# Performance work log

Hardware: AMD Instinct MI355X
Metric: run time of the kernel (lower is better)

The kernel has to match this reference:

```python
import jax, jax.numpy as jnp
import numpy as np

DS = 32   # self_obs_dim
DO = 32   # obstacle_obs_dim
D = DS + DO
H = 128   # obstacle_hidden_size
B = 512   # batch_size
A = 16    # num_adv_obs = 2 * num_oppo_obs


def _init_linear(key, fan_in, fan_out):
    kw, kb = jax.random.split(key)
    bound = 1.0 / np.sqrt(fan_in)
    w = jax.random.uniform(kw, (fan_in, fan_out), jnp.float32, -bound, bound)
    b = jax.random.uniform(kb, (fan_out,), jnp.float32, -bound, bound)
    return w, b


def setup_inputs() -> dict:
    key = jax.random.key(0)
    ks = jax.random.split(key, 10)
    obs = jax.random.normal(ks[0], (B, DS), jnp.float32)
    latent = jax.random.normal(ks[1], (B, A, DO), jnp.float32)
    hw1, hb1 = _init_linear(ks[2], D, H)
    hw2, hb2 = _init_linear(ks[3], H, D * H)
    vw1, vb1 = _init_linear(ks[4], H, H)
    vw2, vb2 = _init_linear(ks[5], H, H)
    aw1, ab1 = _init_linear(ks[6], 2 * H, H)
    aw2, ab2 = _init_linear(ks[7], H, H)
    aw3, ab3 = _init_linear(ks[8], H, 1)
    return {
        "obs": obs, "obs_intention_latent": latent,
        "hw1": hw1, "hb1": hb1, "hw2": hw2, "hb2": hb2,
        "vw1": vw1, "vb1": vb1, "vw2": vw2, "vb2": vb2,
        "aw1": aw1, "ab1": ab1, "aw2": aw2, "ab2": ab2,
        "aw3": aw3, "ab3": ab3,
        "num_adv_obs": A, "batch_size": B, "num_groups": 1,
    }


def reference(obs, obs_intention_latent, hw1, hb1, hw2, hb2,
              vw1, vb1, vw2, vb2, aw1, ab1, aw2, ab2, aw3, ab3,
              num_adv_obs, batch_size, num_groups):
    relu = jax.nn.relu
    # flatten opponents (batch-major, matches torch .reshape)
    obs_obstacles = obs_intention_latent.reshape(-1, DO)          # [N, DO]
    # torch .repeat(num_adv_obs, 1) tiles the batch dim
    self_rep = jnp.tile(obs[:, :DS], (num_adv_obs, 1))            # [N, DS]
    mlp_input = jnp.concatenate([self_rep, obs_obstacles], axis=1)  # [N, D]
    # hypernet: per-sample weight [N, D, H]
    h = relu(mlp_input @ hw1 + hb1)
    w = relu(h @ hw2 + hb2).reshape(-1, D, H)
    # per-sample vector-matrix product + tanh
    emb = jnp.tanh(jnp.einsum("nd,ndh->nh", mlp_input, w))        # [N, H]
    # neighbor value MLP
    vals = relu(relu(emb @ vw1 + vb1) @ vw2 + vb2)                # [N, H]
    # attention: concat with per-batch mean embedding
    emb_mean = jnp.mean(emb.reshape(batch_size, -1, H), axis=1)   # [B, H]
    mean_rep = jnp.tile(emb_mean, (num_adv_obs, 1))               # [N, H]
    att_in = jnp.concatenate([emb, mean_rep], axis=1)             # [N, 2H]
    scores = relu(relu(att_in @ aw1 + ab1) @ aw2 + ab2) @ aw3 + ab3  # [N, 1]
    att = jax.nn.softmax(scores.reshape(batch_size, -1), axis=1).reshape(-1, 1)
    weighted = (att * vals).reshape(batch_size, -1, H)
    return jnp.sum(weighted, axis=1)                              # [B, H]
```

## Files before the change

### kernel.cpp

```cpp
#include <hip/hip_runtime.h>
#include <hip/hip_bf16.h>
#include <math.h>

#define BATCH 512
#define NADV  16
#define NROWS (BATCH*NADV)
#define DS    32
#define DO    32
#define DIM   64
#define HID   128
#define WCOLS (DIM*HID)
#define LSTR  136
#define PACK_BLOCKS 276

typedef _Float16 half8 __attribute__((ext_vector_type(8)));
typedef float floatx4 __attribute__((ext_vector_type(4)));

__device__ inline void async_ld16(void* lds, const void* g) {
    __builtin_amdgcn_global_load_lds(
        (const __attribute__((address_space(1))) void*)g,
        (__attribute__((address_space(3))) void*)lds, 16, 0, 0);
}

__global__ __launch_bounds__(256)
void k_prep(const float* __restrict__ obs, const float* __restrict__ latent,
            const float* __restrict__ hw1, const float* __restrict__ hb1,
            const float* __restrict__ hw2, const float* __restrict__ vw1,
            const float* __restrict__ vw2, const float* __restrict__ aw1,
            const float* __restrict__ aw2,
            _Float16* __restrict__ hf,
            _Float16* __restrict__ w2p, _Float16* __restrict__ vw1p,
            _Float16* __restrict__ vw2p, _Float16* __restrict__ aw1p,
            _Float16* __restrict__ aw2p) {
    __shared__ __align__(16) float smem[32 * 132];
    int b = blockIdx.x;
    int tid = threadIdx.x;
    if (b < PACK_BLOCKS) {
        const float* src; _Float16* dst; int N, Kt, jb, kt;
        if (b < 256)      { src = hw2; dst = w2p;  N = WCOLS; Kt = 4; jb = b >> 2; kt = b & 3; }
        else if (b < 260) { src = vw1; dst = vw1p; N = HID;   Kt = 4; jb = 0; kt = b - 256; }
        else if (b < 264) { src = vw2; dst = vw2p; N = HID;   Kt = 4; jb = 0; kt = b - 260; }
        else if (b < 272) { src = aw1; dst = aw1p; N = HID;   Kt = 8; jb = 0; kt = b - 264; }
        else              { src = aw2; dst = aw2p; N = HID;   Kt = 4; jb = 0; kt = b - 272; }
        for (int i = tid; i < 32 * 32; i += 256) {
            int r = i >> 5, c4 = (i & 31) * 4;
            *(float4*)&smem[r * 132 + c4] =
                *(const float4*)(src + (size_t)(kt * 32 + r) * N + jb * 128 + c4);
        }
        __syncthreads();
        for (int i = tid; i < 8 * 64; i += 256) {
            int ctl = i >> 6, lane = i & 63;
            int ct = jb * 8 + ctl;
            int rbase = (lane >> 4) * 8, cc = ctl * 16 + (lane & 15);
            half8 v;
#pragma unroll
            for (int e = 0; e < 8; ++e) v[e] = (_Float16)smem[(rbase + e) * 132 + cc];
            *(half8*)(dst + ((size_t)ct * Kt + kt) * 512 + lane * 8) = v;
        }
    } else {
        int n0 = (b - PACK_BLOCKS) * 16;
        float* xs = smem;
        for (int idx = tid; idx < 16 * DIM; idx += 256) {
            int r = idx >> 6, d = idx & 63;
            int n = n0 + r;
            xs[r * DIM + d] = (d < DS) ? obs[(n & (BATCH - 1)) * DS + d]
                                       : latent[(size_t)n * DO + (d - DS)];
        }
        __syncthreads();
        int j = tid & 127, hh = tid >> 7;
        float acc[8];
        float bb = hb1[j];
#pragma unroll
        for (int r = 0; r < 8; ++r) acc[r] = bb;
        for (int d = 0; d < DIM; ++d) {
            float w = hw1[d * HID + j];
#pragma unroll
            for (int r = 0; r < 8; ++r)
                acc[r] = fmaf(xs[(hh * 8 + r) * DIM + d], w, acc[r]);
        }
#pragma unroll
        for (int r = 0; r < 8; ++r)
            hf[(size_t)(n0 + hh * 8 + r) * HID + j] = (_Float16)fmaxf(acc[r], 0.f);
    }
}

__global__ __launch_bounds__(512, 4)
void k_hyper_mfma(const float* __restrict__ obs, const float* __restrict__ latent,
                  const _Float16* __restrict__ hf, const _Float16* __restrict__ w2p,
                  const float* __restrict__ hb2,
                  _Float16* __restrict__ embf, _Float16* __restrict__ emeanf) {
    __shared__ __align__(16) _Float16 Bs[8][4][512];
    __shared__ float xs[128][68];
    __shared__ float bias_s[64 * 16];
    int b  = blockIdx.x;
    int jt = b & 7;
    int rt = b >> 3;
    int n0 = rt * 128;
    int j0 = jt * 16;
    int tid = threadIdx.x;
    int wave = tid >> 6, lane = tid & 63;
    int l15 = lane & 15, quad = lane >> 4;

    for (int i = tid; i < 128 * 16; i += 512) {
        int r = i >> 4, c4 = (i & 15) * 4;
        float4 v;
        if (c4 < DS) v = *(const float4*)(obs + ((n0 + r) & (BATCH - 1)) * DS + c4);
        else         v = *(const float4*)(latent + (size_t)(n0 + r) * DO + (c4 - DS));
        *(float4*)&xs[r][c4] = v;
    }
    for (int i = tid; i < 64 * 16; i += 512)
        bias_s[i] = hb2[(i >> 4) * HID + j0 + (i & 15)];

    half8 af[4];
    {
        const _Float16* arow = hf + (size_t)(n0 + wave * 16 + l15) * HID;
#pragma unroll
        for (int ks = 0; ks < 4; ++ks)
            af[ks] = *(const half8*)(arow + ks * 32 + quad * 8);
    }

    float emb_acc[4] = {0.f, 0.f, 0.f, 0.f};

    for (int d8 = 0; d8 < 8; ++d8) {
        {
            int ct = (d8 * 8 + wave) * 8 + jt;
            const _Float16* src = w2p + (size_t)ct * 2048 + lane * 8;
            _Float16* dst = &Bs[wave][0][0];
#pragma unroll
            for (int kt = 0; kt < 4; ++kt)
                async_ld16(dst + kt * 512, src + kt * 512);
        }
        __syncthreads();

#pragma unroll
        for (int dd = 0; dd < 8; ++dd) {
            int d = d8 * 8 + dd;
            float bb = bias_s[d * 16 + l15];
            floatx4 acc = {bb, bb, bb, bb};
#pragma unroll
            for (int ks = 0; ks < 4; ++ks) {
                half8 bfr = *(const half8*)&Bs[dd][ks][lane * 8];
                acc = __builtin_amdgcn_mfma_f32_16x16x32_f16(af[ks], bfr, acc, 0, 0, 0);
            }
#pragma unroll
            for (int reg = 0; reg < 4; ++reg) {
                float xv = xs[wave * 16 + quad * 4 + reg][d];
                emb_acc[reg] = fmaf(xv, fmaxf(acc[reg], 0.f), emb_acc[reg]);
            }
        }
        __syncthreads();
    }

    float e[4];
#pragma unroll
    for (int reg = 0; reg < 4; ++reg) {
        e[reg] = tanhf(emb_acc[reg]);
        embf[(size_t)(n0 + wave * 16 + quad * 4 + reg) * HID + j0 + l15] =
            (_Float16)e[reg];
    }
    float s = e[0] + e[1] + e[2] + e[3];
    s += __shfl_xor(s, 16, 64);
    s += __shfl_xor(s, 32, 64);
    if (quad == 0)
        emeanf[(size_t)(rt * 8 + wave) * HID + j0 + l15] = (_Float16)(s * (1.f / 16));
}

__global__ __launch_bounds__(512, 4)
void k_tail(const _Float16* __restrict__ embf, const _Float16* __restrict__ emeanf,
            const _Float16* __restrict__ vw1p, const float* __restrict__ vb1,
            const _Float16* __restrict__ vw2p, const float* __restrict__ vb2,
            const _Float16* __restrict__ aw1p, const float* __restrict__ ab1,
            const _Float16* __restrict__ aw2p, const float* __restrict__ ab2,
            const float* __restrict__ aw3, const float* __restrict__ ab3,
            float* __restrict__ out) {
    __shared__ _Float16 embs[16][LSTR];
    __shared__ _Float16 means[16][LSTR];
    __shared__ _Float16 tAs[16][LSTR];
    __shared__ _Float16 tBs[16][LSTR];
    __shared__ float scr[16][32];
    __shared__ float satt[16];
    __shared__ float att[16];
    int g = blockIdx.x;
    int n0 = g * 16;
    int tid = threadIdx.x;
    int wave = tid >> 6, lane = tid & 63, l15 = lane & 15, quad = lane >> 4;
    int ct = wave;

    {
        int m = tid >> 8, r = (tid >> 4) & 15, c8 = (tid & 15) * 8;
        if (m == 0)
            *(half8*)&embs[r][c8] = *(const half8*)(embf + (size_t)(n0 + r) * HID + c8);
        else
            *(half8*)&means[r][c8] =
                *(const half8*)(emeanf + (size_t)((n0 & 511) + r) * HID + c8);
    }
    __syncthreads();

    half8 av[4], amean[4];
#pragma unroll
    for (int ks = 0; ks < 4; ++ks) {
        av[ks]    = *(const half8*)&embs[l15][ks * 32 + quad * 8];
        amean[ks] = *(const half8*)&means[l15][ks * 32 + quad * 8];
    }

    floatx4 acc;
    {
        float bb = vb1[ct * 16 + l15];
        acc = (floatx4){bb, bb, bb, bb};
    }
#pragma unroll
    for (int ks = 0; ks < 4; ++ks) {
        half8 bfr = *(const half8*)(vw1p + ((size_t)ct * 4 + ks) * 512 + lane * 8);
        acc = __builtin_amdgcn_mfma_f32_16x16x32_f16(av[ks], bfr, acc, 0, 0, 0);
    }
#pragma unroll
    for (int reg = 0; reg < 4; ++reg)
        tAs[quad * 4 + reg][ct * 16 + l15] = (_Float16)fmaxf(acc[reg], 0.f);
    __syncthreads();

    half8 at[4];
#pragma unroll
    for (int ks = 0; ks < 4; ++ks)
        at[ks] = *(const half8*)&tAs[l15][ks * 32 + quad * 8];

    floatx4 vacc;
    {
        float bb = vb2[ct * 16 + l15];
        vacc = (floatx4){bb, bb, bb, bb};
    }
#pragma unroll
    for (int ks = 0; ks < 4; ++ks) {
        half8 bfr = *(const half8*)(vw2p + ((size_t)ct * 4 + ks) * 512 + lane * 8);
        vacc = __builtin_amdgcn_mfma_f32_16x16x32_f16(at[ks], bfr, vacc, 0, 0, 0);
    }

    floatx4 aacc;
    {
        float bb = ab1[ct * 16 + l15];
        aacc = (floatx4){bb, bb, bb, bb};
    }
#pragma unroll
    for (int ks = 0; ks < 8; ++ks) {
        half8 bfr = *(const half8*)(aw1p + ((size_t)ct * 8 + ks) * 512 + lane * 8);
        half8 a = (ks < 4) ? av[ks] : amean[ks - 4];
        aacc = __builtin_amdgcn_mfma_f32_16x16x32_f16(a, bfr, aacc, 0, 0, 0);
    }
#pragma unroll
    for (int reg = 0; reg < 4; ++reg)
        tBs[quad * 4 + reg][ct * 16 + l15] = (_Float16)fmaxf(aacc[reg], 0.f);
    __syncthreads();

    half8 aa[4];
#pragma unroll
    for (int ks = 0; ks < 4; ++ks)
        aa[ks] = *(const half8*)&tBs[l15][ks * 32 + quad * 8];

    floatx4 a2acc;
    {
        float bb = ab2[ct * 16 + l15];
        a2acc = (floatx4){bb, bb, bb, bb};
    }
#pragma unroll
    for (int ks = 0; ks < 4; ++ks) {
        half8 bfr = *(const half8*)(aw2p + ((size_t)ct * 4 + ks) * 512 + lane * 8);
        a2acc = __builtin_amdgcn_mfma_f32_16x16x32_f16(aa[ks], bfr, a2acc, 0, 0, 0);
    }
    __syncthreads();
#pragma unroll
    for (int reg = 0; reg < 4; ++reg)
        tAs[quad * 4 + reg][ct * 16 + l15] = (_Float16)fmaxf(a2acc[reg], 0.f);
    __syncthreads();

    {
        int r = tid >> 5, ch = tid & 31;
        float p = 0.f;
#pragma unroll
        for (int k = 0; k < 4; ++k)
            p += (float)tAs[r][ch * 4 + k] * aw3[ch * 4 + k];
        scr[r][ch] = p;
    }
    __syncthreads();
    if (tid < 16) {
        float s = ab3[0];
#pragma unroll
        for (int ch = 0; ch < 32; ++ch) s += scr[tid][ch];
        satt[tid] = s;
    }
    __syncthreads();
    if (tid < 16) {
        float m = -1e30f;
#pragma unroll
        for (int a = 0; a < 16; ++a) m = fmaxf(m, satt[a]);
        float S = 0.f;
#pragma unroll
        for (int a = 0; a < 16; ++a) S += expf(satt[a] - m);
        att[tid] = expf(satt[tid] - m) / S;
    }
    __syncthreads();

    {
        float p = 0.f;
#pragma unroll
        for (int reg = 0; reg < 4; ++reg)
            p += att[quad * 4 + reg] * fmaxf(vacc[reg], 0.f);
        p += __shfl_xor(p, 16, 64);
        p += __shfl_xor(p, 32, 64);
        if (quad == 0) out[(size_t)g * HID + ct * 16 + l15] = p;
    }
}

extern "C" void kernel_launch(void* const* d_in, const int* in_sizes, int n_in,
                              void* d_out, int out_size, void* d_ws, size_t ws_size,
                              hipStream_t stream) {
    const float* obs = (const float*)d_in[0];
    const float* lat = (const float*)d_in[1];
    const float* hw1 = (const float*)d_in[2];
    const float* hb1 = (const float*)d_in[3];
    const float* hw2 = (const float*)d_in[4];
    const float* hb2 = (const float*)d_in[5];
    const float* vw1 = (const float*)d_in[6];
    const float* vb1 = (const float*)d_in[7];
    const float* vw2 = (const float*)d_in[8];
    const float* vb2 = (const float*)d_in[9];
    const float* aw1 = (const float*)d_in[10];
    const float* ab1 = (const float*)d_in[11];
    const float* aw2 = (const float*)d_in[12];
    const float* ab2 = (const float*)d_in[13];
    const float* aw3 = (const float*)d_in[14];
    const float* ab3 = (const float*)d_in[15];
    float* out = (float*)d_out;

    char* ws = (char*)d_ws;
    _Float16*  hf     = (_Float16*)ws;  ws += (size_t)NROWS * HID * 2;
    _Float16*  w2p    = (_Float16*)ws;  ws += (size_t)WCOLS * HID * 2;
    _Float16*  embf   = (_Float16*)ws;  ws += (size_t)NROWS * HID * 2;
    _Float16*  emeanf = (_Float16*)ws;  ws += (size_t)BATCH * HID * 2;
    _Float16*  vw1p   = (_Float16*)ws;  ws += (size_t)HID * HID * 2;
    _Float16*  vw2p   = (_Float16*)ws;  ws += (size_t)HID * HID * 2;
    _Float16*  aw1p   = (_Float16*)ws;  ws += (size_t)2 * HID * HID * 2;
    _Float16*  aw2p   = (_Float16*)ws;  ws += (size_t)HID * HID * 2;

    hipLaunchKernelGGL(k_prep, dim3(PACK_BLOCKS + NROWS / 16), dim3(256), 0, stream,
                       obs, lat, hw1, hb1, hw2, vw1, vw2, aw1, aw2,
                       hf, w2p, vw1p, vw2p, aw1p, aw2p);
    hipLaunchKernelGGL(k_hyper_mfma, dim3(512), dim3(512), 0, stream,
                       obs, lat, hf, w2p, hb2, embf, emeanf);
    hipLaunchKernelGGL(k_tail, dim3(BATCH), dim3(512), 0, stream,
                       embf, emeanf, vw1p, vb1, vw2p, vb2,
                       aw1p, ab1, aw2p, ab2, aw3, ab3, out);
}
```

Before: 132.1 us.

## Double-buffer hypernet weight staging and streamline tail kernel score reduction

The hypernet MFMA kernel now double-buffers the async LDS staging of the W2 tiles, so the next tile loads while the current one is computed. The x-input and bias staging through shared memory is removed; those values are now read straight from global memory into registers. The tail kernel loads its embedding and mean fragments directly from global memory. It also replaces the multi-barrier shared-memory score and softmax reduction with a single-wave shuffle reduction, which cuts syncthreads. In exchange, LDS use for Bs doubles and redundant global loads of x and the bias increase.

```diff
diff --git a/kernel.cpp b/kernel.cpp
--- a/kernel.cpp
+++ b/kernel.cpp
@@ -89,9 +89,7 @@
                   const _Float16* __restrict__ hf, const _Float16* __restrict__ w2p,
                   const float* __restrict__ hb2,
                   _Float16* __restrict__ embf, _Float16* __restrict__ emeanf) {
-    __shared__ __align__(16) _Float16 Bs[8][4][512];
-    __shared__ float xs[128][68];
-    __shared__ float bias_s[64 * 16];
+    __shared__ __align__(16) _Float16 Bs[2][8][4][512];
     int b  = blockIdx.x;
     int jt = b & 7;
     int rt = b >> 3;
@@ -100,16 +98,7 @@
     int tid = threadIdx.x;
     int wave = tid >> 6, lane = tid & 63;
     int l15 = lane & 15, quad = lane >> 4;
-
-    for (int i = tid; i < 128 * 16; i += 512) {
-        int r = i >> 4, c4 = (i & 15) * 4;
-        float4 v;
-        if (c4 < DS) v = *(const float4*)(obs + ((n0 + r) & (BATCH - 1)) * DS + c4);
-        else         v = *(const float4*)(latent + (size_t)(n0 + r) * DO + (c4 - DS));
-        *(float4*)&xs[r][c4] = v;
-    }
-    for (int i = tid; i < 64 * 16; i += 512)
-        bias_s[i] = hb2[(i >> 4) * HID + j0 + (i & 15)];
+    int row_lo = n0 + wave * 16 + quad * 4;
 
     half8 af[4];
     {
@@ -119,36 +108,52 @@
             af[ks] = *(const half8*)(arow + ks * 32 + quad * 8);
     }
 
+    auto stage = [&](int d8, int buf) {
+        int ct = (d8 * 8 + wave) * 8 + jt;
+        const _Float16* src = w2p + (size_t)ct * 2048 + lane * 8;
+        _Float16* dst = &Bs[buf][wave][0][0];
+#pragma unroll
+        for (int kt = 0; kt < 4; ++kt)
+            async_ld16(dst + kt * 512, src + kt * 512);
+    };
+
+    stage(0, 0);
+
     float emb_acc[4] = {0.f, 0.f, 0.f, 0.f};
 
+#pragma unroll
     for (int d8 = 0; d8 < 8; ++d8) {
-        {
-            int ct = (d8 * 8 + wave) * 8 + jt;
-            const _Float16* src = w2p + (size_t)ct * 2048 + lane * 8;
-            _Float16* dst = &Bs[wave][0][0];
-#pragma unroll
-            for (int kt = 0; kt < 4; ++kt)
-                async_ld16(dst + kt * 512, src + kt * 512);
-        }
+        int cur = d8 & 1;
         __syncthreads();
+        if (d8 < 7) stage(d8 + 1, cur ^ 1);
+
+        float xr[4][8];
+#pragma unroll
+        for (int r = 0; r < 4; ++r) {
+            int row = row_lo + r;
+            const float* p = (d8 < 4)
+                ? obs + (size_t)(row & (BATCH - 1)) * DS + d8 * 8
+                : latent + (size_t)row * DO + (d8 - 4) * 8;
+            float4 t0 = *(const float4*)p;
+            float4 t1 = *(const float4*)(p + 4);
+            xr[r][0] = t0.x; xr[r][1] = t0.y; xr[r][2] = t0.z; xr[r][3] = t0.w;
+            xr[r][4] = t1.x; xr[r][5] = t1.y; xr[r][6] = t1.z; xr[r][7] = t1.w;
+        }
 
 #pragma unroll
         for (int dd = 0; dd < 8; ++dd) {
             int d = d8 * 8 + dd;
-            float bb = bias_s[d * 16 + l15];
+            float bb = hb2[d * HID + j0 + l15];
             floatx4 acc = {bb, bb, bb, bb};
 #pragma unroll
             for (int ks = 0; ks < 4; ++ks) {
-                half8 bfr = *(const half8*)&Bs[dd][ks][lane * 8];
+                half8 bfr = *(const half8*)&Bs[cur][dd][ks][lane * 8];
                 acc = __builtin_amdgcn_mfma_f32_16x16x32_f16(af[ks], bfr, acc, 0, 0, 0);
             }
 #pragma unroll
-            for (int reg = 0; reg < 4; ++reg) {
-                float xv = xs[wave * 16 + quad * 4 + reg][d];
-                emb_acc[reg] = fmaf(xv, fmaxf(acc[reg], 0.f), emb_acc[reg]);
-            }
-        }
-        __syncthreads();
+            for (int reg = 0; reg < 4; ++reg)
+                emb_acc[reg] = fmaf(xr[reg][dd], fmaxf(acc[reg], 0.f), emb_acc[reg]);
+        }
     }
 
     float e[4];
@@ -173,12 +178,9 @@
             const _Float16* __restrict__ aw2p, const float* __restrict__ ab2,
             const float* __restrict__ aw3, const float* __restrict__ ab3,
             float* __restrict__ out) {
-    __shared__ _Float16 embs[16][LSTR];
-    __shared__ _Float16 means[16][LSTR];
     __shared__ _Float16 tAs[16][LSTR];
     __shared__ _Float16 tBs[16][LSTR];
-    __shared__ float scr[16][32];
-    __shared__ float satt[16];
+    __shared__ _Float16 tCs[16][LSTR];
     __shared__ float att[16];
     int g = blockIdx.x;
     int n0 = g * 16;
@@ -186,21 +188,15 @@
     int wave = tid >> 6, lane = tid & 63, l15 = lane & 15, quad = lane >> 4;
     int ct = wave;
 
-    {
-        int m = tid >> 8, r = (tid >> 4) & 15, c8 = (tid & 15) * 8;
-        if (m == 0)
-            *(half8*)&embs[r][c8] = *(const half8*)(embf + (size_t)(n0 + r) * HID + c8);
-        else
-            *(half8*)&means[r][c8] =
-                *(const half8*)(emeanf + (size_t)((n0 & 511) + r) * HID + c8);
-    }
-    __syncthreads();
-
     half8 av[4], amean[4];
-#pragma unroll
-    for (int ks = 0; ks < 4; ++ks) {
-        av[ks]    = *(const half8*)&embs[l15][ks * 32 + quad * 8];
-        amean[ks] = *(const half8*)&means[l15][ks * 32 + quad * 8];
+    {
+        const _Float16* erow = embf + (size_t)(n0 + l15) * HID;
+        const _Float16* mrow = emeanf + (size_t)((n0 + l15) & (BATCH - 1)) * HID;
+#pragma unroll
+        for (int ks = 0; ks < 4; ++ks) {
+            av[ks]    = *(const half8*)(erow + ks * 32 + quad * 8);
+            amean[ks] = *(const half8*)(mrow + ks * 32 + quad * 8);
+        }
     }
 
     floatx4 acc;
@@ -265,36 +261,35 @@
         half8 bfr = *(const half8*)(aw2p + ((size_t)ct * 4 + ks) * 512 + lane * 8);
         a2acc = __builtin_amdgcn_mfma_f32_16x16x32_f16(aa[ks], bfr, a2acc, 0, 0, 0);
     }
+#pragma unroll
+    for (int reg = 0; reg < 4; ++reg)
+        tCs[quad * 4 + reg][ct * 16 + l15] = (_Float16)fmaxf(a2acc[reg], 0.f);
     __syncthreads();
-#pragma unroll
-    for (int reg = 0; reg < 4; ++reg)
-        tAs[quad * 4 + reg][ct * 16 + l15] = (_Float16)fmaxf(a2acc[reg], 0.f);
-    __syncthreads();
-
-    {
-        int r = tid >> 5, ch = tid & 31;
+
+    if (wave == 0) {
+        int r = lane >> 2, q4 = lane & 3;
         float p = 0.f;
 #pragma unroll
-        for (int k = 0; k < 4; ++k)
-            p += (float)tAs[r][ch * 4 + k] * aw3[ch * 4 + k];
-        scr[r][ch] = p;
-    }
-    __syncthreads();
-    if (tid < 16) {
-        float s = ab3[0];
-#pragma unroll
-        for (int ch = 0; ch < 32; ++ch) s += scr[tid][ch];
-        satt[tid] = s;
-    }
-    __syncthreads();
-    if (tid < 16) {
-        float m = -1e30f;
-#pragma unroll
-        for (int a = 0; a < 16; ++a) m = fmaxf(m, satt[a]);
-        float S = 0.f;
-#pragma unroll
-        for (int a = 0; a < 16; ++a) S += expf(satt[a] - m);
-        att[tid] = expf(satt[tid] - m) / S;
+        for (int c = 0; c < 4; ++c) {
+            half8 v = *(const half8*)&tCs[r][q4 * 32 + c * 8];
+            float4 w0 = *(const float4*)(aw3 + q4 * 32 + c * 8);
+            float4 w1 = *(const float4*)(aw3 + q4 * 32 + c * 8 + 4);
+            p += (float)v[0] * w0.x + (float)v[1] * w0.y +
+                 (float)v[2] * w0.z + (float)v[3] * w0.w +
+                 (float)v[4] * w1.x + (float)v[5] * w1.y +
+                 (float)v[6] * w1.z + (float)v[7] * w1.w;
+        }
+        p += __shfl_xor(p, 1, 64);
+        p += __shfl_xor(p, 2, 64);
+        float s = p + ab3[0];
+        float m = s;
+#pragma unroll
+        for (int off = 4; off < 64; off <<= 1) m = fmaxf(m, __shfl_xor(m, off, 64));
+        float e = expf(s - m);
+        float S = e;
+#pragma unroll
+        for (int off = 4; off < 64; off <<= 1) S += __shfl_xor(S, off, 64);
+        if (q4 == 0) att[r] = e / S;
     }
     __syncthreads();
 
```

Result: slower. 141.9 us (+7.4%).
